# Performance work log

Measured on AMD Instinct MI355X. Metric: run time of the kernel, lower is better.

Reference implementation:

```python
import jax, jax.numpy as jnp
import numpy as np

N = 50000      # nodes
E = 800000     # edges (avg degree 16)
DIN = 128
DH = 128
DOUT = 40
ALPHA = 0.1
BETA = 1.0


def gcn_conv(x, src, dst, ew, W, b, n):
    """PyG GCNConv: add self-loops, symmetric deg^-1/2 normalization, gather-scatter."""
    idx = jnp.arange(n)
    s = jnp.concatenate([src, idx])
    d = jnp.concatenate([dst, idx])
    w = jnp.concatenate([ew, jnp.ones((n,), x.dtype)])
    deg = jax.ops.segment_sum(w, d, num_segments=n)            # [N]
    dinv = jnp.where(deg > 0, jax.lax.rsqrt(deg), 0.0)
    norm = dinv[s] * w * dinv[d]                               # [E+N]
    h = x @ W                                                  # [N, dout]
    msg = h[s] * norm[:, None]                                 # gather + scale
    out = jax.ops.segment_sum(msg, d, num_segments=n)          # scatter-add
    return out + b


def setup_inputs() -> dict:
    key = jax.random.key(0)
    ks = jax.random.split(key, 10)
    x = jax.random.normal(ks[0], (N, DIN), jnp.float32)
    edge_index = jax.random.randint(ks[1], (2, E), 0, N, dtype=jnp.int64)
    edge_weight = jax.random.uniform(ks[2], (E,), jnp.float32)
    W1 = jax.random.normal(ks[3], (DIN, DH), jnp.float32) / np.float32(np.sqrt(DIN))
    b1 = jnp.zeros((DH,), jnp.float32)
    W2 = jax.random.normal(ks[4], (DH, DH), jnp.float32) / np.float32(np.sqrt(DH))
    b2 = jnp.zeros((DH,), jnp.float32)
    W3 = jax.random.normal(ks[5], (DH, DOUT), jnp.float32) / np.float32(np.sqrt(DH))
    b3 = jnp.zeros((DOUT,), jnp.float32)
    return {"x": x, "edge_index": edge_index, "edge_weight": edge_weight,
            "W1": W1, "b1": b1, "W2": W2, "b2": b2, "W3": W3, "b3": b3}


def reference(x, edge_index, edge_weight, W1, b1, W2, b2, W3, b3):
    src, dst = edge_index[0], edge_index[1]
    ones_w = jnp.ones((E,), x.dtype)
    h1 = jax.nn.relu(gcn_conv(x, src, dst, ones_w, W1, b1, N))   # conv1 (edge_weight=None)
    hc = gcn_conv(h1, src, dst, edge_weight, W2, b2, N)          # crf_layer with edge_weight
    h = ALPHA * h1 + BETA * hc                                   # weighted residual combo
    # LearnableBernoulliDropout: identity in eval mode
    out = gcn_conv(h, src, dst, ones_w, W3, b3, N)               # conv2
    return jax.nn.log_softmax(out, axis=1)
```

## Files before the change

kernel.cpp:

```cpp
#include <hip/hip_runtime.h>
#include <math.h>

#define DIN  128
#define DH   128
#define DOUT 40
#define ALPHA_C 0.1f
#define BETA_C  1.0f
#define SLOT 64

#define NPB 512
#define NPB_SHIFT 9
#define MAXBK 128
#define BCAP 12288

typedef __attribute__((ext_vector_type(8))) short short8;
typedef __attribute__((ext_vector_type(4))) float floatx4;

static inline int cdiv_h(int a, int b) { return (a + b - 1) / b; }

static __device__ __forceinline__ unsigned short f2b(float f) {
    unsigned u = __float_as_uint(f);
    u = u + 0x7FFFu + ((u >> 16) & 1u);
    return (unsigned short)(u >> 16);
}
static __device__ __forceinline__ unsigned pk2(float x, float y) {
    return (unsigned)f2b(x) | ((unsigned)f2b(y) << 16);
}
static __device__ __forceinline__ float2 b2f2(unsigned u) {
    float2 r;
    r.x = __uint_as_float(u << 16);
    r.y = __uint_as_float(u & 0xFFFF0000u);
    return r;
}

__global__ __launch_bounds__(256) void init_gcur(int* __restrict__ gcur, int nbk) {
    int b = threadIdx.x;
    if (b < nbk) gcur[b] = b * BCAP;
}

__global__ __launch_bounds__(256) void bucket_p1(const int* __restrict__ src,
                                                 const int* __restrict__ dst,
                                                 const float* __restrict__ ew,
                                                 int* __restrict__ gcur,
                                                 int2* __restrict__ stage,
                                                 int E, int nbk) {
    __shared__ int hist[MAXBK], off[MAXBK], sbase[MAXBK];
    int t = threadIdx.x;
    int nb = gridDim.x;
    int C = (E + nb - 1) / nb;
    int e0 = blockIdx.x * C;
    int e1 = e0 + C; if (e1 > E) e1 = E;

    for (int i = t; i < nbk; i += 256) { hist[i] = 0; off[i] = 0; }
    __syncthreads();
    for (int e = e0 + t; e < e1; e += 256)
        atomicAdd(&hist[dst[e] >> NPB_SHIFT], 1);
    __syncthreads();
    for (int i = t; i < nbk; i += 256)
        sbase[i] = atomicAdd(&gcur[i], hist[i]);
    __syncthreads();
    for (int e = e0 + t; e < e1; e += 256) {
        int d = dst[e];
        int b = d >> NPB_SHIFT;
        int pos = atomicAdd(&off[b], 1);
        int idx = sbase[b] + pos;
        if (idx < (b + 1) * BCAP) {
            int2 v;
            v.x = (src[e] & 0xFFFF) | ((d & (NPB - 1)) << 16);
            v.y = __float_as_int(ew[e]);
            stage[idx] = v;
        }
    }
}

__global__ __launch_bounds__(256) void bucket_p2(const int2* __restrict__ stage,
                                                 const int* __restrict__ gcur,
                                                 int2* __restrict__ csr,
                                                 int* __restrict__ cnt,
                                                 float* __restrict__ dinv1,
                                                 float* __restrict__ dinv2, int Nn) {
    __shared__ int   lcnt[NPB];
    __shared__ float lws[NPB];
    int b = blockIdx.x;
    int t = threadIdx.x;
    for (int i = t; i < NPB; i += 256) { lcnt[i] = 0; lws[i] = 0.f; }
    __syncthreads();

    int base = b * BCAP;
    int n = gcur[b] - base; if (n > BCAP) n = BCAP;
    for (int i = t; i < n; i += 256) {
        int2 v = stage[base + i];
        int dl = (v.x >> 16) & (NPB - 1);
        int pos = atomicAdd(&lcnt[dl], 1);
        atomicAdd(&lws[dl], __int_as_float(v.y));
        if (pos < SLOT) {
            int d = (b << NPB_SHIFT) + dl;
            int2 o; o.x = v.x & 0xFFFF; o.y = v.y;
            csr[(d << 6) + pos] = o;
        }
    }
    __syncthreads();

    int d0 = b << NPB_SHIFT;
    for (int i = t; i < NPB; i += 256) {
        int d = d0 + i;
        if (d < Nn) {
            int c = lcnt[i]; if (c > SLOT) c = SLOT;
            cnt[d] = c;
            dinv1[d] = rsqrtf((float)c + 1.f);
            dinv2[d] = rsqrtf(1.f + lws[i]);
        }
    }
}

template <bool ABF16>
__global__ __launch_bounds__(256) void gemm128(const void* __restrict__ Ain,
                                               const float* __restrict__ W,
                                               unsigned short* __restrict__ C, int M) {
    __shared__ short As[128 * 128];
    __shared__ short Bs[128 * 128];
    int t = threadIdx.x;
    int blockM = blockIdx.x * 128;

    {
        int r = t >> 1, h = t & 1;
        int rg = blockM + r; if (rg > M - 1) rg = M - 1;
        if (ABF16) {
            const uint4* arow = (const uint4*)((const unsigned short*)Ain + (size_t)rg * 128);
            #pragma unroll
            for (int i = 0; i < 8; ++i) {
                int chunk = h * 8 + i;
                uint4 v = arow[chunk];
                *(uint4*)&As[r * 128 + ((chunk ^ (r & 7)) * 8)] = v;
            }
        } else {
            const float4* arow = (const float4*)((const float*)Ain + (size_t)rg * 128);
            #pragma unroll
            for (int i = 0; i < 8; ++i) {
                int chunk = h * 8 + i;
                float4 v0 = arow[chunk * 2], v1 = arow[chunk * 2 + 1];
                uint4 p;
                p.x = pk2(v0.x, v0.y); p.y = pk2(v0.z, v0.w);
                p.z = pk2(v1.x, v1.y); p.w = pk2(v1.z, v1.w);
                *(uint4*)&As[r * 128 + ((chunk ^ (r & 7)) * 8)] = p;
            }
        }
    }
    {
        int n = t & 127;
        int k0 = (t >> 7) * 64;
        #pragma unroll
        for (int it = 0; it < 8; ++it) {
            int k = k0 + it * 8;
            float f0 = W[(size_t)(k + 0) * 128 + n];
            float f1 = W[(size_t)(k + 1) * 128 + n];
            float f2 = W[(size_t)(k + 2) * 128 + n];
            float f3 = W[(size_t)(k + 3) * 128 + n];
            float f4 = W[(size_t)(k + 4) * 128 + n];
            float f5 = W[(size_t)(k + 5) * 128 + n];
            float f6 = W[(size_t)(k + 6) * 128 + n];
            float f7 = W[(size_t)(k + 7) * 128 + n];
            uint4 p;
            p.x = pk2(f0, f1); p.y = pk2(f2, f3);
            p.z = pk2(f4, f5); p.w = pk2(f6, f7);
            *(uint4*)&Bs[n * 128 + (((k >> 3) ^ (n & 7)) * 8)] = p;
        }
    }
    __syncthreads();

    int w = t >> 6, l = t & 63;
    int q = l >> 4, lm = l & 15;
    int rowoff = (w >> 1) * 64, coloff = (w & 1) * 64;

    floatx4 acc[4][4] = {};
    #pragma unroll
    for (int ks = 0; ks < 4; ++ks) {
        int chunk = ks * 4 + q;
        int sw = (chunk ^ (lm & 7)) * 8;
        short8 af[4], bf[4];
        #pragma unroll
        for (int tm = 0; tm < 4; ++tm)
            af[tm] = *(const short8*)&As[(rowoff + tm * 16 + lm) * 128 + sw];
        #pragma unroll
        for (int tn = 0; tn < 4; ++tn)
            bf[tn] = *(const short8*)&Bs[(coloff + tn * 16 + lm) * 128 + sw];
        #pragma unroll
        for (int tm = 0; tm < 4; ++tm)
            #pragma unroll
            for (int tn = 0; tn < 4; ++tn)
                acc[tm][tn] = __builtin_amdgcn_mfma_f32_16x16x32_bf16(af[tm], bf[tn], acc[tm][tn], 0, 0, 0);
    }

    #pragma unroll
    for (int tm = 0; tm < 4; ++tm) {
        #pragma unroll
        for (int reg = 0; reg < 4; ++reg) {
            int row = blockM + rowoff + tm * 16 + q * 4 + reg;
            if (row >= M) continue;
            #pragma unroll
            for (int tn = 0; tn < 4; ++tn) {
                int col = coloff + tn * 16 + lm;
                C[(size_t)row * 128 + col] = f2b(acc[tm][tn][reg]);
            }
        }
    }
}

__global__ __launch_bounds__(256) void gemm40_lsm(const unsigned short* __restrict__ Ain,
                                                  const float* __restrict__ W,
                                                  const float* __restrict__ bias,
                                                  float* __restrict__ out, int M) {
    __shared__ short As[128 * 128];
    __shared__ short Bs[48 * 128];
    int t = threadIdx.x;
    int blockM = blockIdx.x * 128;

    {
        int r = t >> 1, h = t & 1;
        int rg = blockM + r; if (rg > M - 1) rg = M - 1;
        const uint4* arow = (const uint4*)(Ain + (size_t)rg * 128);
        #pragma unroll
        for (int i = 0; i < 8; ++i) {
            int chunk = h * 8 + i;
            uint4 v = arow[chunk];
            *(uint4*)&As[r * 128 + ((chunk ^ (r & 7)) * 8)] = v;
        }
    }
    {
        int n = t & 63;
        int k0 = (t >> 6) * 32;
        #pragma unroll
        for (int it = 0; it < 4; ++it) {
            int k = k0 + it * 8;
            uint4 p = {0, 0, 0, 0};
            if (n < 40) {
                float f0 = W[(size_t)(k + 0) * 40 + n];
                float f1 = W[(size_t)(k + 1) * 40 + n];
                float f2 = W[(size_t)(k + 2) * 40 + n];
                float f3 = W[(size_t)(k + 3) * 40 + n];
                float f4 = W[(size_t)(k + 4) * 40 + n];
                float f5 = W[(size_t)(k + 5) * 40 + n];
                float f6 = W[(size_t)(k + 6) * 40 + n];
                float f7 = W[(size_t)(k + 7) * 40 + n];
                p.x = pk2(f0, f1); p.y = pk2(f2, f3);
                p.z = pk2(f4, f5); p.w = pk2(f6, f7);
            }
            if (n < 48)
                *(uint4*)&Bs[n * 128 + (((k >> 3) ^ (n & 7)) * 8)] = p;
        }
    }
    __syncthreads();

    int w = t >> 6, l = t & 63;
    int q = l >> 4, lm = l & 15;
    int rowoff = w * 32;

    floatx4 acc[2][3] = {};
    #pragma unroll
    for (int ks = 0; ks < 4; ++ks) {
        int chunk = ks * 4 + q;
        int sw = (chunk ^ (lm & 7)) * 8;
        short8 af[2], bf[3];
        #pragma unroll
        for (int tm = 0; tm < 2; ++tm)
            af[tm] = *(const short8*)&As[(rowoff + tm * 16 + lm) * 128 + sw];
        #pragma unroll
        for (int tn = 0; tn < 3; ++tn)
            bf[tn] = *(const short8*)&Bs[(tn * 16 + lm) * 128 + sw];
        #pragma unroll
        for (int tm = 0; tm < 2; ++tm)
            #pragma unroll
            for (int tn = 0; tn < 3; ++tn)
                acc[tm][tn] = __builtin_amdgcn_mfma_f32_16x16x32_bf16(af[tm], bf[tn], acc[tm][tn], 0, 0, 0);
    }

    float bb0 = bias[lm];
    float bb1 = bias[16 + lm];
    float bb2 = (lm < 8) ? bias[32 + lm] : 0.f;
    #pragma unroll
    for (int tm = 0; tm < 2; ++tm) {
        #pragma unroll
        for (int reg = 0; reg < 4; ++reg) {
            int row = blockM + rowoff + tm * 16 + q * 4 + reg;
            float v0 = acc[tm][0][reg] + bb0;
            float v1 = acc[tm][1][reg] + bb1;
            float v2 = (lm < 8) ? acc[tm][2][reg] + bb2 : -INFINITY;
            float mx = fmaxf(fmaxf(v0, v1), v2);
            #pragma unroll
            for (int o = 1; o < 16; o <<= 1) mx = fmaxf(mx, __shfl_xor(mx, o, 64));
            float ss = expf(v0 - mx) + expf(v1 - mx) + ((lm < 8) ? expf(v2 - mx) : 0.f);
            #pragma unroll
            for (int o = 1; o < 16; o <<= 1) ss += __shfl_xor(ss, o, 64);
            float ls = mx + logf(ss);
            if (row < M) {
                out[(size_t)row * 40 + lm]      = v0 - ls;
                out[(size_t)row * 40 + 16 + lm] = v1 - ls;
                if (lm < 8) out[(size_t)row * 40 + 32 + lm] = v2 - ls;
            }
        }
    }
}

template <int MODE>
__global__ __launch_bounds__(256) void agg128(const unsigned short* __restrict__ hpre,
                                              unsigned short* __restrict__ io,
                                              const float* __restrict__ bias,
                                              const float* __restrict__ dinv,
                                              const int* __restrict__ cnt,
                                              const int2* __restrict__ csr, int n) {
    int row = blockIdx.x * 4 + (threadIdx.x >> 6);
    if (row >= n) return;
    int lane = threadIdx.x & 63;
    const unsigned* hp = (const unsigned*)hpre;

    float di = dinv[row];
    float d2 = di * di;
    float2 acc = b2f2(hp[(size_t)row * 64 + lane]);
    if (MODE == 2) {
        acc.x *= d2; acc.y *= d2;
    } else {
        float2 bb = ((const float2*)bias)[lane];
        acc.x = fmaf(acc.x, d2, bb.x);
        acc.y = fmaf(acc.y, d2, bb.y);
    }

    int c = cnt[row]; if (c > SLOT) c = SLOT;
    int jb = row << 6;
    int je = jb + c;
    int j = jb;

    while (j + 8 <= je) {
        int2 ee[8]; float2 ff[8];
        #pragma unroll
        for (int u = 0; u < 8; ++u) ee[u] = csr[j + u];
        #pragma unroll
        for (int u = 0; u < 8; ++u) ff[u] = b2f2(hp[(size_t)ee[u].x * 64 + lane]);
        #pragma unroll
        for (int u = 0; u < 8; ++u) {
            float cc = (MODE == 1) ? dinv[ee[u].x] * __int_as_float(ee[u].y) * di
                                   : dinv[ee[u].x] * di;
            acc.x = fmaf(cc, ff[u].x, acc.x);
            acc.y = fmaf(cc, ff[u].y, acc.y);
        }
        j += 8;
    }
    if (j + 4 <= je) {
        int2 ee[4]; float2 ff[4];
        #pragma unroll
        for (int u = 0; u < 4; ++u) ee[u] = csr[j + u];
        #pragma unroll
        for (int u = 0; u < 4; ++u) ff[u] = b2f2(hp[(size_t)ee[u].x * 64 + lane]);
        #pragma unroll
        for (int u = 0; u < 4; ++u) {
            float cc = (MODE == 1) ? dinv[ee[u].x] * __int_as_float(ee[u].y) * di
                                   : dinv[ee[u].x] * di;
            acc.x = fmaf(cc, ff[u].x, acc.x);
            acc.y = fmaf(cc, ff[u].y, acc.y);
        }
        j += 4;
    }
    for (; j < je; ++j) {
        int2 e0 = csr[j];
        float cc = (MODE == 1) ? dinv[e0.x] * __int_as_float(e0.y) * di
                               : dinv[e0.x] * di;
        float2 f0 = b2f2(hp[(size_t)e0.x * 64 + lane]);
        acc.x = fmaf(cc, f0.x, acc.x);
        acc.y = fmaf(cc, f0.y, acc.y);
    }

    unsigned* iop = (unsigned*)io;
    if (MODE == 0) {
        acc.x = fmaxf(acc.x, 0.f); acc.y = fmaxf(acc.y, 0.f);
        iop[(size_t)row * 64 + lane] = pk2(acc.x, acc.y);
    } else if (MODE == 1) {
        float2 h1 = b2f2(iop[(size_t)row * 64 + lane]);
        acc.x = fmaf(ALPHA_C, h1.x, BETA_C * acc.x);
        acc.y = fmaf(ALPHA_C, h1.y, BETA_C * acc.y);
        iop[(size_t)row * 64 + lane] = pk2(acc.x, acc.y);
    } else {
        iop[(size_t)row * 64 + lane] = pk2(acc.x, acc.y);
    }
}

extern "C" void kernel_launch(void* const* d_in, const int* in_sizes, int n_in,
                              void* d_out, int out_size, void* d_ws, size_t ws_size,
                              hipStream_t stream) {
    const float* x   = (const float*)d_in[0];
    const int*   ei  = (const int*)  d_in[1];
    const float* ew  = (const float*)d_in[2];
    const float* W1  = (const float*)d_in[3];
    const float* b1  = (const float*)d_in[4];
    const float* W2  = (const float*)d_in[5];
    const float* b2  = (const float*)d_in[6];
    const float* W3  = (const float*)d_in[7];
    const float* b3  = (const float*)d_in[8];
    float* out = (float*)d_out;

    const int Nn = in_sizes[0] / DIN;
    const int E  = in_sizes[1] / 2;
    const int* src = ei;
    const int* dst = ei + E;

    char* wsb = (char*)d_ws;
    int*   cnt     = (int*)wsb;                          wsb += (size_t)Nn * 4;
    float* dinv1   = (float*)wsb;                        wsb += (size_t)Nn * 4;
    float* dinv2   = (float*)wsb;                        wsb += (size_t)Nn * 4;
    int2*  csr     = (int2*)wsb;                         wsb += (size_t)Nn * SLOT * 8;
    unsigned short* hpreb = (unsigned short*)wsb;        wsb += (size_t)Nn * DH * 2;
    unsigned short* h1b   = (unsigned short*)wsb;        wsb += (size_t)Nn * DH * 2;
    int*   gcur    = (int*)wsb;                          wsb += (size_t)MAXBK * 4;

    int2* stage = (int2*)hpreb;
    int nbk = cdiv_h(Nn, NPB);

    init_gcur<<<1, 256, 0, stream>>>(gcur, nbk);
    bucket_p1<<<128, 256, 0, stream>>>(src, dst, ew, gcur, stage, E, nbk);
    bucket_p2<<<nbk, 256, 0, stream>>>(stage, gcur, csr, cnt, dinv1, dinv2, Nn);

    int gemmGrid = cdiv_h(Nn, 128);
    int aggGrid = cdiv_h(Nn, 4);

    gemm128<false><<<gemmGrid, 256, 0, stream>>>(x, W1, hpreb, Nn);
    agg128<0><<<aggGrid, 256, 0, stream>>>(hpreb, h1b, b1, dinv1, cnt, csr, Nn);

    gemm128<true><<<gemmGrid, 256, 0, stream>>>(h1b, W2, hpreb, Nn);
    agg128<1><<<aggGrid, 256, 0, stream>>>(hpreb, h1b, b2, dinv2, cnt, csr, Nn);

    agg128<2><<<aggGrid, 256, 0, stream>>>(h1b, hpreb, b3, dinv1, cnt, csr, Nn);
    gemm40_lsm<<<gemmGrid, 256, 0, stream>>>(hpreb, W3, b3, out, Nn);
}
```

Baseline: 280.9 us.

## Reorder final GCN layer to project to 40 dims before aggregation

The last layer now runs the 128→40 GEMM first and then aggregates over neighbours in 40-dim space, with log-softmax fused into the new aggregation kernel. This cuts the gathered bytes per edge from 256 to 80 and removes the 128-wide third aggregation pass. The agg128 template drops its MODE 2 path, and one wavefront per row now leaves 24 of 64 lanes idle. The 80-byte rows are not aligned for wide loads, and the bf16 rounding now happens after the projection instead of before it.

```diff
diff --git a/kernel.cpp b/kernel.cpp
--- a/kernel.cpp
+++ b/kernel.cpp
@@ -31,6 +31,9 @@
     r.x = __uint_as_float(u << 16);
     r.y = __uint_as_float(u & 0xFFFF0000u);
     return r;
+}
+static __device__ __forceinline__ float b2f1(unsigned short u) {
+    return __uint_as_float(((unsigned)u) << 16);
 }
 
 __global__ __launch_bounds__(256) void init_gcur(int* __restrict__ gcur, int nbk) {
@@ -206,10 +209,9 @@
     }
 }
 
-__global__ __launch_bounds__(256) void gemm40_lsm(const unsigned short* __restrict__ Ain,
-                                                  const float* __restrict__ W,
-                                                  const float* __restrict__ bias,
-                                                  float* __restrict__ out, int M) {
+__global__ __launch_bounds__(256) void gemm40(const unsigned short* __restrict__ Ain,
+                                              const float* __restrict__ W,
+                                              unsigned short* __restrict__ Cb, int M) {
     __shared__ short As[128 * 128];
     __shared__ short Bs[48 * 128];
     int t = threadIdx.x;
@@ -274,29 +276,16 @@
                 acc[tm][tn] = __builtin_amdgcn_mfma_f32_16x16x32_bf16(af[tm], bf[tn], acc[tm][tn], 0, 0, 0);
     }
 
-    float bb0 = bias[lm];
-    float bb1 = bias[16 + lm];
-    float bb2 = (lm < 8) ? bias[32 + lm] : 0.f;
     #pragma unroll
     for (int tm = 0; tm < 2; ++tm) {
         #pragma unroll
         for (int reg = 0; reg < 4; ++reg) {
             int row = blockM + rowoff + tm * 16 + q * 4 + reg;
-            float v0 = acc[tm][0][reg] + bb0;
-            float v1 = acc[tm][1][reg] + bb1;
-            float v2 = (lm < 8) ? acc[tm][2][reg] + bb2 : -INFINITY;
-            float mx = fmaxf(fmaxf(v0, v1), v2);
-            #pragma unroll
-            for (int o = 1; o < 16; o <<= 1) mx = fmaxf(mx, __shfl_xor(mx, o, 64));
-            float ss = expf(v0 - mx) + expf(v1 - mx) + ((lm < 8) ? expf(v2 - mx) : 0.f);
-            #pragma unroll
-            for (int o = 1; o < 16; o <<= 1) ss += __shfl_xor(ss, o, 64);
-            float ls = mx + logf(ss);
-            if (row < M) {
-                out[(size_t)row * 40 + lm]      = v0 - ls;
-                out[(size_t)row * 40 + 16 + lm] = v1 - ls;
-                if (lm < 8) out[(size_t)row * 40 + 32 + lm] = v2 - ls;
-            }
+            if (row >= M) continue;
+            Cb[(size_t)row * 40 + lm]      = f2b(acc[tm][0][reg]);
+            Cb[(size_t)row * 40 + 16 + lm] = f2b(acc[tm][1][reg]);
+            if (lm < 8)
+                Cb[(size_t)row * 40 + 32 + lm] = f2b(acc[tm][2][reg]);
         }
     }
 }
@@ -316,9 +305,7 @@
     float di = dinv[row];
     float d2 = di * di;
     float2 acc = b2f2(hp[(size_t)row * 64 + lane]);
-    if (MODE == 2) {
-        acc.x *= d2; acc.y *= d2;
-    } else {
+    {
         float2 bb = ((const float2*)bias)[lane];
         acc.x = fmaf(acc.x, d2, bb.x);
         acc.y = fmaf(acc.y, d2, bb.y);
@@ -372,14 +359,72 @@
     if (MODE == 0) {
         acc.x = fmaxf(acc.x, 0.f); acc.y = fmaxf(acc.y, 0.f);
         iop[(size_t)row * 64 + lane] = pk2(acc.x, acc.y);
-    } else if (MODE == 1) {
+    } else {
         float2 h1 = b2f2(iop[(size_t)row * 64 + lane]);
         acc.x = fmaf(ALPHA_C, h1.x, BETA_C * acc.x);
         acc.y = fmaf(ALPHA_C, h1.y, BETA_C * acc.y);
         iop[(size_t)row * 64 + lane] = pk2(acc.x, acc.y);
-    } else {
-        iop[(size_t)row * 64 + lane] = pk2(acc.x, acc.y);
-    }
+    }
+}
+
+__global__ __launch_bounds__(256) void agg40_lsm(const unsigned short* __restrict__ h40,
+                                                 const float* __restrict__ bias,
+                                                 const float* __restrict__ dinv,
+                                                 const int* __restrict__ cnt,
+                                                 const int2* __restrict__ csr,
+                                                 float* __restrict__ out, int n) {
+    int row = blockIdx.x * 4 + (threadIdx.x >> 6);
+    if (row >= n) return;
+    int lane = threadIdx.x & 63;
+    bool act = lane < 40;
+    int ln = act ? lane : 39;
+
+    float di = dinv[row];
+    float d2 = di * di;
+    float acc = b2f1(h40[(size_t)row * 40 + ln]) * d2;
+
+    int c = cnt[row]; if (c > SLOT) c = SLOT;
+    int jb = row << 6;
+    int je = jb + c;
+    int j = jb;
+
+    while (j + 8 <= je) {
+        int ss[8]; float ff[8];
+        #pragma unroll
+        for (int u = 0; u < 8; ++u) ss[u] = csr[j + u].x;
+        #pragma unroll
+        for (int u = 0; u < 8; ++u) ff[u] = b2f1(h40[(size_t)ss[u] * 40 + ln]);
+        #pragma unroll
+        for (int u = 0; u < 8; ++u)
+            acc = fmaf(dinv[ss[u]] * di, ff[u], acc);
+        j += 8;
+    }
+    if (j + 4 <= je) {
+        int ss[4]; float ff[4];
+        #pragma unroll
+        for (int u = 0; u < 4; ++u) ss[u] = csr[j + u].x;
+        #pragma unroll
+        for (int u = 0; u < 4; ++u) ff[u] = b2f1(h40[(size_t)ss[u] * 40 + ln]);
+        #pragma unroll
+        for (int u = 0; u < 4; ++u)
+            acc = fmaf(dinv[ss[u]] * di, ff[u], acc);
+        j += 4;
+    }
+    for (; j < je; ++j) {
+        int s0 = csr[j].x;
+        acc = fmaf(dinv[s0] * di, b2f1(h40[(size_t)s0 * 40 + ln]), acc);
+    }
+
+    float v = act ? (acc + bias[ln]) : -INFINITY;
+    float mx = v;
+    #pragma unroll
+    for (int o = 1; o < 64; o <<= 1) mx = fmaxf(mx, __shfl_xor(mx, o, 64));
+    float e = act ? expf(v - mx) : 0.f;
+    float ssum = e;
+    #pragma unroll
+    for (int o = 1; o < 64; o <<= 1) ssum += __shfl_xor(ssum, o, 64);
+    float ls = mx + logf(ssum);
+    if (act) out[(size_t)row * 40 + lane] = v - ls;
 }
 
 extern "C" void kernel_launch(void* const* d_in, const int* in_sizes, int n_in,
@@ -426,6 +471,7 @@
     gemm128<true><<<gemmGrid, 256, 0, stream>>>(h1b, W2, hpreb, Nn);
     agg128<1><<<aggGrid, 256, 0, stream>>>(hpreb, h1b, b2, dinv2, cnt, csr, Nn);
 
-    agg128<2><<<aggGrid, 256, 0, stream>>>(h1b, hpreb, b3, dinv1, cnt, csr, Nn);
-    gemm40_lsm<<<gemmGrid, 256, 0, stream>>>(hpreb, W3, b3, out, Nn);
-}
+    unsigned short* h40 = hpreb;
+    gemm40<<<gemmGrid, 256, 0, stream>>>(h1b, W3, h40, Nn);
+    agg40_lsm<<<aggGrid, 256, 0, stream>>>(h40, b3, dinv1, cnt, csr, out, Nn);
+}
```

Measured after the change: 272.8 us. 2.9% less time.
